# Performance work log

Hardware: AMD Instinct MI355X
Metric: run time of the kernel (lower is better)

Reference implementation:

```python
import jax, jax.numpy as jnp
import numpy as np

N_NODES = 100000
N_EDGES = 500000
N_REL = 3
IN_F, HID_F, OUT_F = 128, 128, 128
H_HALF = OUT_F // 2  # BiLSTM hidden per direction


def setup_inputs() -> dict:
    key = jax.random.key(0)
    ks = jax.random.split(key, 16)
    s = 0.05
    inp = {
        "x": jax.random.normal(ks[0], (N_NODES, IN_F), jnp.float32),
        "src": jax.random.randint(ks[1], (N_REL, N_EDGES), 0, N_NODES),
        "dst": jax.random.randint(ks[2], (N_REL, N_EDGES), 0, N_NODES),
        # per-relation GraphConv weights (layer 1 and 2)
        "W1": jax.random.normal(ks[3], (N_REL, IN_F, HID_F), jnp.float32) * s,
        "b1": jnp.zeros((N_REL, HID_F), jnp.float32),
        "W2": jax.random.normal(ks[4], (N_REL, HID_F, OUT_F), jnp.float32) * s,
        "b2": jnp.zeros((N_REL, OUT_F), jnp.float32),
        # BiLSTM (1 layer, seq_len=1); PyTorch gate order i,f,g,o
        "Wih_f": jax.random.normal(ks[5], (4 * H_HALF, OUT_F), jnp.float32) * s,
        "Whh_f": jax.random.normal(ks[6], (4 * H_HALF, H_HALF), jnp.float32) * s,
        "bih_f": jnp.zeros((4 * H_HALF,), jnp.float32),
        "bhh_f": jnp.zeros((4 * H_HALF,), jnp.float32),
        "Wih_b": jax.random.normal(ks[7], (4 * H_HALF, OUT_F), jnp.float32) * s,
        "Whh_b": jax.random.normal(ks[8], (4 * H_HALF, H_HALF), jnp.float32) * s,
        "bih_b": jnp.zeros((4 * H_HALF,), jnp.float32),
        "bhh_b": jnp.zeros((4 * H_HALF,), jnp.float32),
    }
    return inp


def _hetero_conv(x, src, dst, W, b):
    """HeteroGraphConv(GraphConv, norm='both'), mean-aggregated over relations.
    x: [N,Din]; src,dst: [R,E]; W: [R,Din,Dout]; b: [R,Dout] -> [N,Dout]."""
    n = x.shape[0]

    def rel_conv(s, d, w, bb):
        ones = jnp.ones(s.shape[0], x.dtype)
        deg_out = jnp.clip(jax.ops.segment_sum(ones, s, num_segments=n), 1.0)
        deg_in = jnp.clip(jax.ops.segment_sum(ones, d, num_segments=n), 1.0)
        # weight first (in_feats >= out_feats path in DGL); math-equivalent
        xw = (x * jax.lax.rsqrt(deg_out)[:, None]) @ w          # [N,Dout]
        agg = jax.ops.segment_sum(xw[s], d, num_segments=n)     # [N,Dout]
        return agg * jax.lax.rsqrt(deg_in)[:, None] + bb

    outs = jax.vmap(rel_conv)(src, dst, W, b)  # [R,N,Dout]
    return jnp.mean(outs, axis=0)


def _lstm_step(x, Wih, bih, bhh):
    # single LSTM step from zero (h0, c0); Whh contributes nothing
    g = x @ Wih.T + bih + bhh
    i, f, gg, o = jnp.split(g, 4, axis=-1)
    c = jax.nn.sigmoid(i) * jnp.tanh(gg)
    return jax.nn.sigmoid(o) * jnp.tanh(c)


def reference(x, src, dst, W1, b1, W2, b2,
              Wih_f, Whh_f, bih_f, bhh_f,
              Wih_b, Whh_b, bih_b, bhh_b):
    h = jax.nn.relu(_hetero_conv(x, src, dst, W1, b1))
    h = _hetero_conv(h, src, dst, W2, b2)          # [N, OUT_F]
    hf = _lstm_step(h, Wih_f, bih_f, bhh_f)        # [N, H_HALF]
    hb = _lstm_step(h, Wih_b, bih_b, bhh_b)        # [N, H_HALF]
    return jnp.concatenate([hf, hb], axis=-1)      # [N, OUT_F]
```

## Files before the change

kernel.cpp:

```cpp
#include <hip/hip_runtime.h>
#include <hip/hip_fp16.h>
#include <math.h>

#define NN 100000
#define NE 500000
#define NREL 3
#define F 128
#define SCAN_BLK 1024
#define NBLK ((NN + SCAN_BLK - 1) / SCAN_BLK)
#define CH 25000
#define NCH 4

#define RANGE 16384
#define NRANGE 7
#define NPAD (NRANGE * RANGE)
#define EC 20
#define EPC (NE / EC)

typedef __attribute__((ext_vector_type(8))) short bf16x8;
typedef __attribute__((ext_vector_type(4))) float f32x4;

__device__ __forceinline__ float sigm(float x) { return 1.f / (1.f + __expf(-x)); }

__device__ __forceinline__ unsigned bf16rne(float x) {
  unsigned u = __float_as_uint(x);
  return (u + 0x7FFFu + ((u >> 16) & 1u)) >> 16;
}
__device__ __forceinline__ void split1(float x, unsigned& h, unsigned& l) {
  h = bf16rne(x);
  float hf = __uint_as_float(h << 16);
  l = bf16rne(x - hf);
}

__device__ __forceinline__ int swz(int row, int slot) {
  return row * 32 + ((slot ^ ((row >> 1) & 3)) << 3);
}

__global__ __launch_bounds__(256) void hist_part(const int* __restrict__ src,
                                                 const int* __restrict__ dst,
                                                 int* __restrict__ part) {
  int x = blockIdx.x & 7, q = blockIdx.x >> 3;
  int g = q % NRANGE;
  int rc2 = x + 8 * (q / NRANGE);
  int a = rc2 / (NREL * EC);
  int rcl = rc2 % (NREL * EC);
  int r = rcl / EC, c = rcl % EC;
  __shared__ int h[RANGE];
  for (int i = threadIdx.x; i < RANGE; i += 256) h[i] = 0;
  __syncthreads();
  const int* idx = (a ? dst : src) + (size_t)r * NE + (size_t)c * EPC;
  const int4* v4 = (const int4*)idx;
  int lo = g * RANGE;
  for (int i = threadIdx.x; i < EPC / 4; i += 256) {
    int4 v = v4[i];
    int t;
    t = v.x - lo; if ((unsigned)t < RANGE) atomicAdd(&h[t], 1);
    t = v.y - lo; if ((unsigned)t < RANGE) atomicAdd(&h[t], 1);
    t = v.z - lo; if ((unsigned)t < RANGE) atomicAdd(&h[t], 1);
    t = v.w - lo; if ((unsigned)t < RANGE) atomicAdd(&h[t], 1);
  }
  __syncthreads();
  int* op = part + (((size_t)a * NREL + r) * EC + c) * NPAD + (size_t)g * RANGE;
  for (int i = threadIdx.x; i < RANGE; i += 256) op[i] = h[i];
}

__global__ void reduce_part(const int* __restrict__ part, int* __restrict__ cnt_out,
                            int* __restrict__ cnt_in) {
  int i = blockIdx.x * blockDim.x + threadIdx.x;
  if (i >= 2 * NREL * NN) return;
  int a = i / (NREL * NN);
  int rn = i - a * (NREL * NN);
  const int* p = part + ((size_t)a * NREL + rn / NN) * EC * NPAD + (rn % NN);
  int s = 0;
#pragma unroll
  for (int c = 0; c < EC; ++c) s += p[(size_t)c * NPAD];
  (a ? cnt_in : cnt_out)[rn] = s;
}

__global__ void make_rs(const int* __restrict__ cnt_out, const int* __restrict__ cnt_in,
                        float* __restrict__ rs_out, float* __restrict__ rs_in3) {
  int i = blockIdx.x * blockDim.x + threadIdx.x;
  if (i >= NREL * NN) return;
  int c0 = cnt_out[i];
  rs_out[i] = rsqrtf((float)(c0 < 1 ? 1 : c0));
  int c1 = cnt_in[i];
  rs_in3[i] = rsqrtf((float)(c1 < 1 ? 1 : c1)) * (1.f / 3.f);
}

__global__ __launch_bounds__(256) void scan1(const int* __restrict__ cnt,
                                             int* __restrict__ excl, int* __restrict__ bsums) {
  int rb = blockIdx.x;
  int r = rb / NBLK, blk = rb % NBLK;
  int tid = (int)threadIdx.x;
  int v[4]; int sum = 0;
#pragma unroll
  for (int i = 0; i < 4; ++i) {
    int idx = blk * SCAN_BLK + tid * 4 + i;
    int c = (idx < NN) ? cnt[r * NN + idx] : 0;
    v[i] = sum; sum += c;
  }
  __shared__ int ts[256];
  ts[tid] = sum;
  __syncthreads();
  for (int off = 1; off < 256; off <<= 1) {
    int t = (tid >= off) ? ts[tid - off] : 0;
    __syncthreads();
    ts[tid] += t;
    __syncthreads();
  }
  int texcl = tid ? ts[tid - 1] : 0;
#pragma unroll
  for (int i = 0; i < 4; ++i) {
    int idx = blk * SCAN_BLK + tid * 4 + i;
    if (idx < NN) excl[r * NN + idx] = texcl + v[i];
  }
  if (tid == 255) bsums[rb] = ts[255];
}

__global__ __launch_bounds__(128) void scan2(int* __restrict__ bsums) {
  int r = blockIdx.x;
  int tid = (int)threadIdx.x;
  __shared__ int ts[128];
  ts[tid] = (tid < NBLK) ? bsums[r * NBLK + tid] : 0;
  __syncthreads();
  for (int off = 1; off < 128; off <<= 1) {
    int t = (tid >= off) ? ts[tid - off] : 0;
    __syncthreads();
    ts[tid] += t;
    __syncthreads();
  }
  if (tid < NBLK) bsums[r * NBLK + tid] = tid ? ts[tid - 1] : 0;
}

__global__ void scan3(int* __restrict__ row_ptr, const int* __restrict__ bsums) {
  int i = blockIdx.x * blockDim.x + threadIdx.x;
  if (i >= NREL * NN) return;
  int r = i / NN, idx = i - r * NN, blk = idx / SCAN_BLK;
  row_ptr[i] += bsums[r * NBLK + blk];
}

__global__ void chunk_prefix(int* __restrict__ part_dst, const int* __restrict__ row_ptr) {
  int i = blockIdx.x * blockDim.x + threadIdx.x;
  if (i >= NREL * NN) return;
  int r = i / NN, node = i - r * NN;
  int* p = part_dst + (size_t)r * EC * NPAD + node;
  int run = row_ptr[i];
#pragma unroll
  for (int c = 0; c < EC; ++c) {
    int t = p[(size_t)c * NPAD];
    p[(size_t)c * NPAD] = run;
    run += t;
  }
}

__global__ void make_pay(const int* __restrict__ src, const float* __restrict__ rs_out,
                         int2* __restrict__ pay) {
  int i = blockIdx.x * blockDim.x + threadIdx.x;
  if (i >= NREL * NE) return;
  int r = i / NE;
  int s = src[i];
  pay[i] = make_int2(s, __float_as_int(rs_out[r * NN + s]));
}

__global__ __launch_bounds__(256) void place_part(const int* __restrict__ dst,
                                                  const int2* __restrict__ pay,
                                                  const int* __restrict__ part_dst,
                                                  int2* __restrict__ ses) {
  int x = blockIdx.x & 7, q = blockIdx.x >> 3;
  int g = q % NRANGE;
  int rc = x + 8 * (q / NRANGE);
  if (rc >= NREL * EC) return;
  int r = rc / EC, c = rc % EC;
  __shared__ int cur[RANGE];
  const int* pc = part_dst + ((size_t)r * EC + c) * NPAD + (size_t)g * RANGE;
  for (int i = threadIdx.x; i < RANGE; i += 256) cur[i] = pc[i];
  __syncthreads();
  int lo = g * RANGE;
  const int4* d4 = (const int4*)(dst + (size_t)r * NE + (size_t)c * EPC);
  const int4* p4 = (const int4*)(pay + (size_t)r * NE + (size_t)c * EPC);
  int2* sesr = ses + (size_t)r * NE;
  for (int i = threadIdx.x; i < EPC / 4; i += 256) {
    int4 dv = d4[i];
    int4 pa = p4[2 * i], pb = p4[2 * i + 1];
    int t;
    t = dv.x - lo; if ((unsigned)t < RANGE) { int pos = atomicAdd(&cur[t], 1); sesr[pos] = make_int2(pa.x, pa.y); }
    t = dv.y - lo; if ((unsigned)t < RANGE) { int pos = atomicAdd(&cur[t], 1); sesr[pos] = make_int2(pa.z, pa.w); }
    t = dv.z - lo; if ((unsigned)t < RANGE) { int pos = atomicAdd(&cur[t], 1); sesr[pos] = make_int2(pb.x, pb.y); }
    t = dv.w - lo; if ((unsigned)t < RANGE) { int pos = atomicAdd(&cur[t], 1); sesr[pos] = make_int2(pb.z, pb.w); }
  }
}

__global__ void prep_small(const float* __restrict__ b1, const float* __restrict__ b2,
                           const float* __restrict__ bif, const float* __restrict__ bhf,
                           const float* __restrict__ bib, const float* __restrict__ bhb,
                           float* __restrict__ bbar1, float* __restrict__ bbar2,
                           float* __restrict__ bselw) {
  int t = (int)threadIdx.x;
  if (t < 128) {
    bbar1[t] = (b1[t] + b1[128 + t] + b1[256 + t]) * (1.f / 3.f);
  } else if (t < 256) {
    int j = t - 128;
    bbar2[j] = (b2[j] + b2[128 + j] + b2[256 + j]) * (1.f / 3.f);
  } else if (t < 640) {
    int m = t - 256;
    int g = m >> 7, j = m & 127, dir = j >> 6, jj = j & 63;
    int grow = (g == 0) ? jj : (g == 1) ? (128 + jj) : (192 + jj);
    bselw[m] = dir ? (bib[grow] + bhb[grow]) : (bif[grow] + bhf[grow]);
  }
}

__global__ void wt_split(const float* __restrict__ W, ushort* __restrict__ th,
                         ushort* __restrict__ tl) {
  int i = blockIdx.x * blockDim.x + threadIdx.x;
  if (i >= 128 * 384) return;
  int n = i / 384, k = i % 384;
  float v = W[(size_t)k * 128 + n];
  unsigned h, l; split1(v, h, l);
  th[i] = (ushort)h; tl[i] = (ushort)l;
}

__global__ void pack_w_split(const float* __restrict__ Wf, const float* __restrict__ Wb,
                             ushort* __restrict__ ph, ushort* __restrict__ pl) {
  int i = blockIdx.x * blockDim.x + threadIdx.x;
  if (i >= 384 * 128) return;
  int m = i / 128, k = i % 128;
  int g = m >> 7, j = m & 127, dir = j >> 6, jj = j & 63;
  int grow = (g == 0) ? jj : (g == 1) ? (128 + jj) : (192 + jj);
  float v = (dir ? Wb : Wf)[(size_t)grow * 128 + k];
  unsigned h, l; split1(v, h, l);
  ph[i] = (ushort)h; pl[i] = (ushort)l;
}

__global__ void cvt_f16(const float* __restrict__ in, ushort* __restrict__ o16) {
  int i = blockIdx.x * blockDim.x + threadIdx.x;
  if (i >= NN * (F / 4)) return;
  float4 v = ((const float4*)in)[i];
  __half2 a = __floats2half2_rn(v.x, v.y);
  __half2 b = __floats2half2_rn(v.z, v.w);
  ((uint2*)o16)[i] = make_uint2(*(unsigned*)&a, *(unsigned*)&b);
}

__global__ __launch_bounds__(256) void gather3(
    const ushort* __restrict__ table, const int2* __restrict__ ses,
    const int* __restrict__ row_ptr, const int* __restrict__ cnt,
    const float* __restrict__ rs_in3, ushort* __restrict__ z16, int n0) {
  int wid = (int)threadIdx.x >> 6, lane = (int)threadIdx.x & 63;
  int gw = blockIdx.x * 4 + wid;
  int r = gw / CH;
  int n = n0 + (gw - r * CH);
  int base = r * NN + n;
  int beg = row_ptr[base], c = cnt[base];
  const int2* el = ses + (size_t)r * NE + beg;
  int half = lane >> 5, cl = lane & 31;
  const uint2* x2 = (const uint2*)table + cl;
  float4 acc = make_float4(0.f, 0.f, 0.f, 0.f);

  int p = 0;
  while (p < c) {
    int rem = c - p; if (rem > 16) rem = 16;
    int2 es = make_int2(0, 0);
    if (lane < rem) es = el[p + lane];
    uint2 rw[8]; float scv[8];
#pragma unroll
    for (int j = 0; j < 8; ++j) {
      int e = 2 * j + half;
      int idx = (e < rem) ? e : 0;
      int s = __shfl(es.x, idx);
      float sc = __int_as_float(__shfl(es.y, idx));
      if (e >= rem) sc = 0.f;
      if (2 * j < rem) {
        rw[j] = x2[(size_t)s * 32];
        scv[j] = sc;
      }
    }
#pragma unroll
    for (int j = 0; j < 8; ++j) {
      if (2 * j < rem) {
        float2 f0 = __half22float2(*(__half2*)&rw[j].x);
        float2 f1 = __half22float2(*(__half2*)&rw[j].y);
        float sc = scv[j];
        acc.x = fmaf(f0.x, sc, acc.x); acc.y = fmaf(f0.y, sc, acc.y);
        acc.z = fmaf(f1.x, sc, acc.z); acc.w = fmaf(f1.y, sc, acc.w);
      }
    }
    p += rem;
  }

  acc.x += __shfl_xor(acc.x, 32);
  acc.y += __shfl_xor(acc.y, 32);
  acc.z += __shfl_xor(acc.z, 32);
  acc.w += __shfl_xor(acc.w, 32);
  if (half == 0) {
    float ci = rs_in3[base];
    __half2 p0 = __floats2half2_rn(acc.x * ci, acc.y * ci);
    __half2 p1 = __floats2half2_rn(acc.z * ci, acc.w * ci);
    size_t zo = (size_t)(n - n0) * 384 + r * 128 + cl * 4;
    *(uint2*)(z16 + zo) = make_uint2(*(unsigned*)&p0, *(unsigned*)&p1);
  }
}

__device__ __forceinline__ void cvt_split8(uint4 v, uint4& hv, uint4& lv) {
  float f[8];
  *(float2*)&f[0] = __half22float2(*(__half2*)&v.x);
  *(float2*)&f[2] = __half22float2(*(__half2*)&v.y);
  *(float2*)&f[4] = __half22float2(*(__half2*)&v.z);
  *(float2*)&f[6] = __half22float2(*(__half2*)&v.w);
  unsigned h[8], l[8];
#pragma unroll
  for (int q = 0; q < 8; ++q) split1(f[q], h[q], l[q]);
  hv = make_uint4(h[0] | (h[1] << 16), h[2] | (h[3] << 16),
                  h[4] | (h[5] << 16), h[6] | (h[7] << 16));
  lv = make_uint4(l[0] | (l[1] << 16), l[2] | (l[3] << 16),
                  l[4] | (l[5] << 16), l[6] | (l[7] << 16));
}

__global__ __launch_bounds__(256) void gemm_mfma1(
    const ushort* __restrict__ z16,
    const ushort* __restrict__ wth, const ushort* __restrict__ wtl,
    const float* __restrict__ bias, ushort* __restrict__ Hout, int n0) {
  __shared__ ushort Ash[64 * 32], Asl[64 * 32], Bsh[128 * 32], Bsl[128 * 32];
  const int row0 = blockIdx.x * 64;
  const int t = (int)threadIdx.x;
  const int wn = t >> 6, l = t & 63, lr = l & 15, lk = l >> 4;
  f32x4 acc[4][2];
#pragma unroll
  for (int a = 0; a < 4; ++a)
#pragma unroll
    for (int b = 0; b < 2; ++b) acc[a][b] = (f32x4){0.f, 0.f, 0.f, 0.f};

  for (int kt = 0; kt < 12; ++kt) {
    __syncthreads();
    {
      int rr = t >> 2, slot = t & 3;
      uint4 v = make_uint4(0, 0, 0, 0);
      if (row0 + rr < CH)
        v = *(const uint4*)(z16 + (size_t)(row0 + rr) * 384 + kt * 32 + slot * 8);
      uint4 hv, lv; cvt_split8(v, hv, lv);
      *(uint4*)&Ash[swz(rr, slot)] = hv;
      *(uint4*)&Asl[swz(rr, slot)] = lv;
    }
#pragma unroll
    for (int i = 0; i < 2; ++i) {
      int s = i * 256 + t;
      int nn_ = s >> 2, slot = s & 3;
      size_t go = (size_t)nn_ * 384 + kt * 32 + slot * 8;
      *(uint4*)&Bsh[swz(nn_, slot)] = *(const uint4*)(wth + go);
      *(uint4*)&Bsl[swz(nn_, slot)] = *(const uint4*)(wtl + go);
    }
    __syncthreads();
    bf16x8 ah[4], al[4], bh[2], bl[2];
#pragma unroll
    for (int mf = 0; mf < 4; ++mf) {
      int off = swz(mf * 16 + lr, lk);
      ah[mf] = *(const bf16x8*)&Ash[off];
      al[mf] = *(const bf16x8*)&Asl[off];
    }
#pragma unroll
    for (int f = 0; f < 2; ++f) {
      int off = swz(wn * 32 + f * 16 + lr, lk);
      bh[f] = *(const bf16x8*)&Bsh[off];
      bl[f] = *(const bf16x8*)&Bsl[off];
    }
#pragma unroll
    for (int mf = 0; mf < 4; ++mf)
#pragma unroll
      for (int f = 0; f < 2; ++f) {
        acc[mf][f] = __builtin_amdgcn_mfma_f32_16x16x32_bf16(ah[mf], bh[f], acc[mf][f], 0, 0, 0);
        acc[mf][f] = __builtin_amdgcn_mfma_f32_16x16x32_bf16(ah[mf], bl[f], acc[mf][f], 0, 0, 0);
        acc[mf][f] = __builtin_amdgcn_mfma_f32_16x16x32_bf16(al[mf], bh[f], acc[mf][f], 0, 0, 0);
      }
  }
#pragma unroll
  for (int mf = 0; mf < 4; ++mf)
#pragma unroll
    for (int f = 0; f < 2; ++f) {
      int col = wn * 32 + f * 16 + lr;
      float bv = bias[col];
#pragma unroll
      for (int reg = 0; reg < 4; ++reg) {
        int row = row0 + mf * 16 + lk * 4 + reg;
        if (row < CH) {
          float v = fmaxf(acc[mf][f][reg] + bv, 0.f);
          __half hv = __float2half_rn(v);
          Hout[(size_t)(n0 + row) * 128 + col] = *(ushort*)&hv;
        }
      }
    }
}

__global__ __launch_bounds__(512) void gemm2_lstm(
    const ushort* __restrict__ z16,
    const ushort* __restrict__ wth, const ushort* __restrict__ wtl,
    const ushort* __restrict__ wph, const ushort* __restrict__ wpl,
    const float* __restrict__ bbar2, const float* __restrict__ bselw,
    float* __restrict__ out, int n0) {
  __shared__ ushort lds[40960];
  ushort* A1h = lds;
  ushort* A1l = lds + 2048;
  ushort* B1h = lds + 4096;
  ushort* B1l = lds + 8192;
  ushort* A2h = lds;
  ushort* A2l = lds + 8192;
  ushort* B3h = lds + 16384;
  ushort* B3l = lds + 28672;

  const int row0 = blockIdx.x * 64;
  const int t = (int)threadIdx.x;
  const int wid = t >> 6, l = t & 63, lr = l & 15, lk = l >> 4;

  f32x4 acc1[4];
#pragma unroll
  for (int a = 0; a < 4; ++a) acc1[a] = (f32x4){0.f, 0.f, 0.f, 0.f};

  for (int kt = 0; kt < 12; ++kt) {
    __syncthreads();
    if (t < 256) {
      int rr = t >> 2, slot = t & 3;
      uint4 v = make_uint4(0, 0, 0, 0);
      if (row0 + rr < CH)
        v = *(const uint4*)(z16 + (size_t)(row0 + rr) * 384 + kt * 32 + slot * 8);
      uint4 hv, lv; cvt_split8(v, hv, lv);
      *(uint4*)&A1h[swz(rr, slot)] = hv;
      *(uint4*)&A1l[swz(rr, slot)] = lv;
    }
    {
      int nn_ = t >> 2, slot = t & 3;
      size_t go = (size_t)nn_ * 384 + kt * 32 + slot * 8;
      *(uint4*)&B1h[swz(nn_, slot)] = *(const uint4*)(wth + go);
      *(uint4*)&B1l[swz(nn_, slot)] = *(const uint4*)(wtl + go);
    }
    __syncthreads();
    bf16x8 ah[4], al[4];
#pragma unroll
    for (int mf = 0; mf < 4; ++mf) {
      int off = swz(mf * 16 + lr, lk);
      ah[mf] = *(const bf16x8*)&A1h[off];
      al[mf] = *(const bf16x8*)&A1l[off];
    }
    int offb = swz(wid * 16 + lr, lk);
    bf16x8 bh = *(const bf16x8*)&B1h[offb];
    bf16x8 bl = *(const bf16x8*)&B1l[offb];
#pragma unroll
    for (int mf = 0; mf < 4; ++mf) {
      acc1[mf] = __builtin_amdgcn_mfma_f32_16x16x32_bf16(ah[mf], bh, acc1[mf], 0, 0, 0);
      acc1[mf] = __builtin_amdgcn_mfma_f32_16x16x32_bf16(ah[mf], bl, acc1[mf], 0, 0, 0);
      acc1[mf] = __builtin_amdgcn_mfma_f32_16x16x32_bf16(al[mf], bh, acc1[mf], 0, 0, 0);
    }
  }

  __syncthreads();
  {
    int colc = wid * 16 + lr;
    float bb = bbar2[colc];
#pragma unroll
    for (int mf = 0; mf < 4; ++mf)
#pragma unroll
      for (int reg = 0; reg < 4; ++reg) {
        int rowc = mf * 16 + lk * 4 + reg;
        float v = acc1[mf][reg] + bb;
        unsigned h, lo2; split1(v, h, lo2);
        int sl2 = (colc >> 3) ^ (rowc & 7);
        int addr = rowc * 128 + (sl2 << 3) + (colc & 7);
        A2h[addr] = (ushort)h;
        A2l[addr] = (ushort)lo2;
      }
  }
  __syncthreads();

  const int wm = wid >> 2, wn3 = wid & 3;
  f32x4 acc3[2][6];
#pragma unroll
  for (int a = 0; a < 2; ++a)
#pragma unroll
    for (int b = 0; b < 6; ++b) acc3[a][b] = (f32x4){0.f, 0.f, 0.f, 0.f};

  for (int kt = 0; kt < 4; ++kt) {
    if (kt) __syncthreads();
#pragma unroll
    for (int i = 0; i < 3; ++i) {
      int s = i * 512 + t;
      int m = s >> 2, slot = s & 3;
      size_t go = (size_t)m * 128 + kt * 32 + slot * 8;
      *(uint4*)&B3h[swz(m, slot)] = *(const uint4*)(wph + go);
      *(uint4*)&B3l[swz(m, slot)] = *(const uint4*)(wpl + go);
    }
    __syncthreads();
    bf16x8 ah2[2], al2[2];
#pragma unroll
    for (int mf = 0; mf < 2; ++mf) {
      int row = wm * 32 + mf * 16 + lr;
      int kslot = kt * 4 + lk;
      int sl2 = kslot ^ (row & 7);
      int addr = row * 128 + (sl2 << 3);
      ah2[mf] = *(const bf16x8*)&A2h[addr];
      al2[mf] = *(const bf16x8*)&A2l[addr];
    }
#pragma unroll
    for (int tt = 0; tt < 6; ++tt) {
      int m = (wn3 + 4 * tt) * 16 + lr;
      int off = swz(m, lk);
      bf16x8 bh = *(const bf16x8*)&B3h[off];
      bf16x8 bl = *(const bf16x8*)&B3l[off];
#pragma unroll
      for (int mf = 0; mf < 2; ++mf) {
        acc3[mf][tt] = __builtin_amdgcn_mfma_f32_16x16x32_bf16(ah2[mf], bh, acc3[mf][tt], 0, 0, 0);
        acc3[mf][tt] = __builtin_amdgcn_mfma_f32_16x16x32_bf16(ah2[mf], bl, acc3[mf][tt], 0, 0, 0);
        acc3[mf][tt] = __builtin_amdgcn_mfma_f32_16x16x32_bf16(al2[mf], bh, acc3[mf][tt], 0, 0, 0);
      }
    }
  }

  int j0 = wn3 * 16 + lr, j1 = j0 + 64;
  float bi0 = bselw[j0], bg0 = bselw[128 + j0], bo0 = bselw[256 + j0];
  float bi1 = bselw[j1], bg1 = bselw[128 + j1], bo1 = bselw[256 + j1];
#pragma unroll
  for (int mf = 0; mf < 2; ++mf)
#pragma unroll
    for (int reg = 0; reg < 4; ++reg) {
      int grow = wm * 32 + mf * 16 + lk * 4 + reg;
      if (row0 + grow < CH) {
        size_t orow = (size_t)(n0 + row0 + grow) * 128;
        float iv0 = acc3[mf][0][reg] + bi0, gv0 = acc3[mf][2][reg] + bg0,
              ov0 = acc3[mf][4][reg] + bo0;
        float c0 = sigm(iv0) * tanhf(gv0);
        out[orow + j0] = sigm(ov0) * tanhf(c0);
        float iv1 = acc3[mf][1][reg] + bi1, gv1 = acc3[mf][3][reg] + bg1,
              ov1 = acc3[mf][5][reg] + bo1;
        float c1 = sigm(iv1) * tanhf(gv1);
        out[orow + j1] = sigm(ov1) * tanhf(c1);
      }
    }
}

extern "C" void kernel_launch(void* const* d_in, const int* in_sizes, int n_in,
                              void* d_out, int out_size, void* d_ws, size_t ws_size,
                              hipStream_t stream) {
  const float* x = (const float*)d_in[0];
  const int* src = (const int*)d_in[1];
  const int* dst = (const int*)d_in[2];
  const float* W1 = (const float*)d_in[3];
  const float* b1 = (const float*)d_in[4];
  const float* W2 = (const float*)d_in[5];
  const float* b2 = (const float*)d_in[6];
  const float* Wih_f = (const float*)d_in[7];
  const float* bih_f = (const float*)d_in[9];
  const float* bhh_f = (const float*)d_in[10];
  const float* Wih_b = (const float*)d_in[11];
  const float* bih_b = (const float*)d_in[13];
  const float* bhh_b = (const float*)d_in[14];
  float* out = (float*)d_out;

  char* wp = (char*)d_ws;
  float* rs_out = (float*)wp;          wp += (size_t)3 * NN * 4;
  float* rs_in3 = (float*)wp;          wp += (size_t)3 * NN * 4;
  int* cnt_out = (int*)wp;             wp += (size_t)3 * NN * 4;
  int* cnt_in = (int*)wp;              wp += (size_t)3 * NN * 4;
  int* row_ptr = (int*)wp;             wp += (size_t)3 * NN * 4;
  int* bsums = (int*)wp;               wp += 4096;
  int2* ses = (int2*)wp;               wp += (size_t)3 * NE * 8;
  ushort* wt1h = (ushort*)wp;          wp += (size_t)128 * 384 * 2;
  ushort* wt1l = (ushort*)wp;          wp += (size_t)128 * 384 * 2;
  ushort* wt2h = (ushort*)wp;          wp += (size_t)128 * 384 * 2;
  ushort* wt2l = (ushort*)wp;          wp += (size_t)128 * 384 * 2;
  ushort* wph = (ushort*)wp;           wp += (size_t)384 * 128 * 2;
  ushort* wpl = (ushort*)wp;           wp += (size_t)384 * 128 * 2;
  float* bbar1 = (float*)wp;           wp += 512;
  float* bbar2 = (float*)wp;           wp += 512;
  float* bselw = (float*)wp;           wp += 2048;
  ushort* z16 = (ushort*)wp;           wp += (size_t)CH * 384 * 2;
  ushort* x16 = (ushort*)wp;           wp += (size_t)NN * F * 2;
  ushort* h116 = (ushort*)wp;          wp += (size_t)NN * F * 2;

  int* part = (int*)z16;
  int* part_dst = part + (size_t)NREL * EC * NPAD;
  int2* pay = (int2*)((char*)h116 + ((size_t)12 << 20));

  hist_part<<<2 * NREL * EC * NRANGE, 256, 0, stream>>>(src, dst, part);
  reduce_part<<<(2 * NREL * NN + 255) / 256, 256, 0, stream>>>(part, cnt_out, cnt_in);
  make_rs<<<(NREL * NN + 255) / 256, 256, 0, stream>>>(cnt_out, cnt_in, rs_out, rs_in3);
  scan1<<<NREL * NBLK, 256, 0, stream>>>(cnt_in, row_ptr, bsums);
  scan2<<<NREL, 128, 0, stream>>>(bsums);
  scan3<<<(NREL * NN + 255) / 256, 256, 0, stream>>>(row_ptr, bsums);
  chunk_prefix<<<(NREL * NN + 255) / 256, 256, 0, stream>>>(part_dst, row_ptr);
  make_pay<<<(NREL * NE + 255) / 256, 256, 0, stream>>>(src, rs_out, pay);
  place_part<<<8 * ((NREL * EC + 7) / 8) * NRANGE, 256, 0, stream>>>(dst, pay, part_dst, ses);

  prep_small<<<1, 640, 0, stream>>>(b1, b2, bih_f, bhh_f, bih_b, bhh_b, bbar1, bbar2, bselw);
  wt_split<<<192, 256, 0, stream>>>(W1, wt1h, wt1l);
  wt_split<<<192, 256, 0, stream>>>(W2, wt2h, wt2l);
  pack_w_split<<<192, 256, 0, stream>>>(Wih_f, Wih_b, wph, wpl);
  cvt_f16<<<(NN * 32 + 255) / 256, 256, 0, stream>>>(x, x16);

  for (int c = 0; c < NCH; ++c) {
    gather3<<<3 * CH / 4, 256, 0, stream>>>(x16, ses, row_ptr, cnt_in, rs_in3, z16, c * CH);
    gemm_mfma1<<<(CH + 63) / 64, 256, 0, stream>>>(z16, wt1h, wt1l, bbar1, h116, c * CH);
  }
  for (int c = 0; c < NCH; ++c) {
    gather3<<<3 * CH / 4, 256, 0, stream>>>(h116, ses, row_ptr, cnt_in, rs_in3, z16, c * CH);
    gemm2_lstm<<<(CH + 63) / 64, 512, 0, stream>>>(z16, wt2h, wt2l, wph, wpl,
                                                   bbar2, bselw, out, c * CH);
  }
}
```

Measured before the change: 520.0 us.

## Shrink histogram partials to ushort, fuse preprocessing kernels, widen gather loads

Per-chunk histogram partials are now stored as 16-bit values, which halves the bytes written and read for degree counting. The reduce and rsqrt kernels are merged into one, and the scan fixup is merged with the chunk prefix, which removes launches and intermediate buffers. The gather kernel now has each lane load 16-byte rows and handle four edges per wave step instead of two, at the cost of eight accumulators and an extra shuffle-reduction stage. Partial counts must fit in 16 bits, which holds for a chunk size of 25000 edges.

```diff
diff --git a/kernel.cpp b/kernel.cpp
--- a/kernel.cpp
+++ b/kernel.cpp
@@ -38,7 +38,7 @@
 
 __global__ __launch_bounds__(256) void hist_part(const int* __restrict__ src,
                                                  const int* __restrict__ dst,
-                                                 int* __restrict__ part) {
+                                                 ushort* __restrict__ part) {
   int x = blockIdx.x & 7, q = blockIdx.x >> 3;
   int g = q % NRANGE;
   int rc2 = x + 8 * (q / NRANGE);
@@ -60,31 +60,26 @@
     t = v.w - lo; if ((unsigned)t < RANGE) atomicAdd(&h[t], 1);
   }
   __syncthreads();
-  int* op = part + (((size_t)a * NREL + r) * EC + c) * NPAD + (size_t)g * RANGE;
-  for (int i = threadIdx.x; i < RANGE; i += 256) op[i] = h[i];
-}
-
-__global__ void reduce_part(const int* __restrict__ part, int* __restrict__ cnt_out,
-                            int* __restrict__ cnt_in) {
-  int i = blockIdx.x * blockDim.x + threadIdx.x;
-  if (i >= 2 * NREL * NN) return;
-  int a = i / (NREL * NN);
-  int rn = i - a * (NREL * NN);
-  const int* p = part + ((size_t)a * NREL + rn / NN) * EC * NPAD + (rn % NN);
-  int s = 0;
-#pragma unroll
-  for (int c = 0; c < EC; ++c) s += p[(size_t)c * NPAD];
-  (a ? cnt_in : cnt_out)[rn] = s;
-}
-
-__global__ void make_rs(const int* __restrict__ cnt_out, const int* __restrict__ cnt_in,
-                        float* __restrict__ rs_out, float* __restrict__ rs_in3) {
+  ushort* op = part + (((size_t)a * NREL + r) * EC + c) * NPAD + (size_t)g * RANGE;
+  for (int i = threadIdx.x; i < RANGE; i += 256) op[i] = (ushort)h[i];
+}
+
+__global__ void reduce_rs(const ushort* __restrict__ part, int* __restrict__ cnt_in,
+                          float* __restrict__ rs_out, float* __restrict__ rs_in3) {
   int i = blockIdx.x * blockDim.x + threadIdx.x;
   if (i >= NREL * NN) return;
-  int c0 = cnt_out[i];
-  rs_out[i] = rsqrtf((float)(c0 < 1 ? 1 : c0));
-  int c1 = cnt_in[i];
-  rs_in3[i] = rsqrtf((float)(c1 < 1 ? 1 : c1)) * (1.f / 3.f);
+  int r = i / NN, node = i - r * NN;
+  const ushort* p0 = part + ((size_t)r * EC) * NPAD + node;
+  const ushort* p1 = part + (((size_t)NREL + r) * EC) * NPAD + node;
+  int s0 = 0, s1 = 0;
+#pragma unroll
+  for (int c = 0; c < EC; ++c) {
+    s0 += p0[(size_t)c * NPAD];
+    s1 += p1[(size_t)c * NPAD];
+  }
+  cnt_in[i] = s1;
+  rs_out[i] = rsqrtf((float)(s0 < 1 ? 1 : s0));
+  rs_in3[i] = rsqrtf((float)(s1 < 1 ? 1 : s1)) * (1.f / 3.f);
 }
 
 __global__ __launch_bounds__(256) void scan1(const int* __restrict__ cnt,
@@ -132,24 +127,19 @@
   if (tid < NBLK) bsums[r * NBLK + tid] = tid ? ts[tid - 1] : 0;
 }
 
-__global__ void scan3(int* __restrict__ row_ptr, const int* __restrict__ bsums) {
+__global__ void scan3_chunk(int* __restrict__ row_ptr, const int* __restrict__ bsums,
+                            const ushort* __restrict__ part, int* __restrict__ cb) {
   int i = blockIdx.x * blockDim.x + threadIdx.x;
   if (i >= NREL * NN) return;
-  int r = i / NN, idx = i - r * NN, blk = idx / SCAN_BLK;
-  row_ptr[i] += bsums[r * NBLK + blk];
-}
-
-__global__ void chunk_prefix(int* __restrict__ part_dst, const int* __restrict__ row_ptr) {
-  int i = blockIdx.x * blockDim.x + threadIdx.x;
-  if (i >= NREL * NN) return;
-  int r = i / NN, node = i - r * NN;
-  int* p = part_dst + (size_t)r * EC * NPAD + node;
-  int run = row_ptr[i];
+  int r = i / NN, node = i - r * NN, blk = node / SCAN_BLK;
+  int base = row_ptr[i] + bsums[r * NBLK + blk];
+  row_ptr[i] = base;
+  const ushort* p1 = part + (((size_t)NREL + r) * EC) * NPAD + node;
+  int run = base;
 #pragma unroll
   for (int c = 0; c < EC; ++c) {
-    int t = p[(size_t)c * NPAD];
-    p[(size_t)c * NPAD] = run;
-    run += t;
+    cb[((size_t)r * EC + c) * NPAD + node] = run;
+    run += p1[(size_t)c * NPAD];
   }
 }
 
@@ -164,7 +154,7 @@
 
 __global__ __launch_bounds__(256) void place_part(const int* __restrict__ dst,
                                                   const int2* __restrict__ pay,
-                                                  const int* __restrict__ part_dst,
+                                                  const int* __restrict__ cb,
                                                   int2* __restrict__ ses) {
   int x = blockIdx.x & 7, q = blockIdx.x >> 3;
   int g = q % NRANGE;
@@ -172,7 +162,7 @@
   if (rc >= NREL * EC) return;
   int r = rc / EC, c = rc % EC;
   __shared__ int cur[RANGE];
-  const int* pc = part_dst + ((size_t)r * EC + c) * NPAD + (size_t)g * RANGE;
+  const int* pc = cb + ((size_t)r * EC + c) * NPAD + (size_t)g * RANGE;
   for (int i = threadIdx.x; i < RANGE; i += 256) cur[i] = pc[i];
   __syncthreads();
   int lo = g * RANGE;
@@ -251,51 +241,59 @@
   int base = r * NN + n;
   int beg = row_ptr[base], c = cnt[base];
   const int2* el = ses + (size_t)r * NE + beg;
-  int half = lane >> 5, cl = lane & 31;
-  const uint2* x2 = (const uint2*)table + cl;
-  float4 acc = make_float4(0.f, 0.f, 0.f, 0.f);
+  int qw = lane >> 4, cl = lane & 15;
+  const uint4* x4 = (const uint4*)table + cl;
+  float acc[8] = {};
 
   int p = 0;
   while (p < c) {
     int rem = c - p; if (rem > 16) rem = 16;
     int2 es = make_int2(0, 0);
     if (lane < rem) es = el[p + lane];
-    uint2 rw[8]; float scv[8];
-#pragma unroll
-    for (int j = 0; j < 8; ++j) {
-      int e = 2 * j + half;
+    uint4 rw[4]; float scv[4];
+#pragma unroll
+    for (int j = 0; j < 4; ++j) {
+      int e = 4 * j + qw;
       int idx = (e < rem) ? e : 0;
       int s = __shfl(es.x, idx);
       float sc = __int_as_float(__shfl(es.y, idx));
       if (e >= rem) sc = 0.f;
-      if (2 * j < rem) {
-        rw[j] = x2[(size_t)s * 32];
+      if (4 * j < rem) {
+        rw[j] = x4[(size_t)s * 16];
         scv[j] = sc;
       }
     }
 #pragma unroll
-    for (int j = 0; j < 8; ++j) {
-      if (2 * j < rem) {
+    for (int j = 0; j < 4; ++j) {
+      if (4 * j < rem) {
+        float sc = scv[j];
         float2 f0 = __half22float2(*(__half2*)&rw[j].x);
         float2 f1 = __half22float2(*(__half2*)&rw[j].y);
-        float sc = scv[j];
-        acc.x = fmaf(f0.x, sc, acc.x); acc.y = fmaf(f0.y, sc, acc.y);
-        acc.z = fmaf(f1.x, sc, acc.z); acc.w = fmaf(f1.y, sc, acc.w);
+        float2 f2 = __half22float2(*(__half2*)&rw[j].z);
+        float2 f3 = __half22float2(*(__half2*)&rw[j].w);
+        acc[0] = fmaf(f0.x, sc, acc[0]); acc[1] = fmaf(f0.y, sc, acc[1]);
+        acc[2] = fmaf(f1.x, sc, acc[2]); acc[3] = fmaf(f1.y, sc, acc[3]);
+        acc[4] = fmaf(f2.x, sc, acc[4]); acc[5] = fmaf(f2.y, sc, acc[5]);
+        acc[6] = fmaf(f3.x, sc, acc[6]); acc[7] = fmaf(f3.y, sc, acc[7]);
       }
     }
     p += rem;
   }
 
-  acc.x += __shfl_xor(acc.x, 32);
-  acc.y += __shfl_xor(acc.y, 32);
-  acc.z += __shfl_xor(acc.z, 32);
-  acc.w += __shfl_xor(acc.w, 32);
-  if (half == 0) {
+#pragma unroll
+  for (int q = 0; q < 8; ++q) {
+    acc[q] += __shfl_xor(acc[q], 16);
+    acc[q] += __shfl_xor(acc[q], 32);
+  }
+  if (qw == 0) {
     float ci = rs_in3[base];
-    __half2 p0 = __floats2half2_rn(acc.x * ci, acc.y * ci);
-    __half2 p1 = __floats2half2_rn(acc.z * ci, acc.w * ci);
-    size_t zo = (size_t)(n - n0) * 384 + r * 128 + cl * 4;
-    *(uint2*)(z16 + zo) = make_uint2(*(unsigned*)&p0, *(unsigned*)&p1);
+    __half2 p0 = __floats2half2_rn(acc[0] * ci, acc[1] * ci);
+    __half2 p1 = __floats2half2_rn(acc[2] * ci, acc[3] * ci);
+    __half2 p2 = __floats2half2_rn(acc[4] * ci, acc[5] * ci);
+    __half2 p3 = __floats2half2_rn(acc[6] * ci, acc[7] * ci);
+    size_t zo = (size_t)(n - n0) * 384 + r * 128 + cl * 8;
+    *(uint4*)(z16 + zo) = make_uint4(*(unsigned*)&p0, *(unsigned*)&p1,
+                                     *(unsigned*)&p2, *(unsigned*)&p3);
   }
 }
 
@@ -553,7 +551,6 @@
   char* wp = (char*)d_ws;
   float* rs_out = (float*)wp;          wp += (size_t)3 * NN * 4;
   float* rs_in3 = (float*)wp;          wp += (size_t)3 * NN * 4;
-  int* cnt_out = (int*)wp;             wp += (size_t)3 * NN * 4;
   int* cnt_in = (int*)wp;              wp += (size_t)3 * NN * 4;
   int* row_ptr = (int*)wp;             wp += (size_t)3 * NN * 4;
   int* bsums = (int*)wp;               wp += 4096;
@@ -571,19 +568,17 @@
   ushort* x16 = (ushort*)wp;           wp += (size_t)NN * F * 2;
   ushort* h116 = (ushort*)wp;          wp += (size_t)NN * F * 2;
 
-  int* part = (int*)z16;
-  int* part_dst = part + (size_t)NREL * EC * NPAD;
+  ushort* part = (ushort*)z16;
+  int* cb = (int*)((char*)z16 + ((size_t)28 << 20));
   int2* pay = (int2*)((char*)h116 + ((size_t)12 << 20));
 
   hist_part<<<2 * NREL * EC * NRANGE, 256, 0, stream>>>(src, dst, part);
-  reduce_part<<<(2 * NREL * NN + 255) / 256, 256, 0, stream>>>(part, cnt_out, cnt_in);
-  make_rs<<<(NREL * NN + 255) / 256, 256, 0, stream>>>(cnt_out, cnt_in, rs_out, rs_in3);
+  reduce_rs<<<(NREL * NN + 255) / 256, 256, 0, stream>>>(part, cnt_in, rs_out, rs_in3);
   scan1<<<NREL * NBLK, 256, 0, stream>>>(cnt_in, row_ptr, bsums);
   scan2<<<NREL, 128, 0, stream>>>(bsums);
-  scan3<<<(NREL * NN + 255) / 256, 256, 0, stream>>>(row_ptr, bsums);
-  chunk_prefix<<<(NREL * NN + 255) / 256, 256, 0, stream>>>(part_dst, row_ptr);
+  scan3_chunk<<<(NREL * NN + 255) / 256, 256, 0, stream>>>(row_ptr, bsums, part, cb);
   make_pay<<<(NREL * NE + 255) / 256, 256, 0, stream>>>(src, rs_out, pay);
-  place_part<<<8 * ((NREL * EC + 7) / 8) * NRANGE, 256, 0, stream>>>(dst, pay, part_dst, ses);
+  place_part<<<8 * ((NREL * EC + 7) / 8) * NRANGE, 256, 0, stream>>>(dst, pay, cb, ses);
 
   prep_small<<<1, 640, 0, stream>>>(b1, b2, bih_f, bhh_f, bih_b, bhh_b, bbar1, bbar2, bselw);
   wt_split<<<192, 256, 0, stream>>>(W1, wt1h, wt1l);
```

Measured after the change: 513.6 us. No clear change (-1.2%).
